# Kernel tuning notes

Hardware: AMD Instinct MI355X
Metric: run time of the kernel (lower is better)

## Reference

```python
import jax, jax.numpy as jnp
import numpy as np

DIM = 8          # per-head dim
ATT_EPS = 1e-15  # LiteMLA eps
BN_EPS = 1e-5    # torch BatchNorm2d default eps


def conv2d(x, w, groups=1, pad=0):
    # x: NCHW, w: OIHW
    return jax.lax.conv_general_dilated(
        x, w, window_strides=(1, 1), padding=[(pad, pad), (pad, pad)],
        dimension_numbers=('NCHW', 'OIHW', 'NCHW'), feature_group_count=groups)


def setup_inputs() -> dict:
    key = jax.random.key(0)
    ks = jax.random.split(key, 6)
    B, C, H, W = 4, 128, 128, 128
    heads = C // DIM            # 16
    t3 = 3 * C                  # 3*total_dim = 384
    x = jax.random.normal(ks[0], (B, C, H, W), jnp.float32)
    w_qkv = jax.random.normal(ks[1], (t3, C, 1, 1), jnp.float32) * 0.02
    w_dw = jax.random.normal(ks[2], (t3, 1, 5, 5), jnp.float32) * 0.02      # depthwise 5x5
    w_pw = jax.random.normal(ks[3], (t3, t3 // (3 * heads), 1, 1), jnp.float32) * 0.05  # grouped 1x1, groups=3*heads
    w_proj = jax.random.normal(ks[4], (C, 2 * C, 1, 1), jnp.float32) * 0.02  # proj 1x1: 2C -> C
    bn_gamma = jnp.ones((C,), jnp.float32)
    bn_beta = jnp.zeros((C,), jnp.float32)
    bn_mean = jnp.zeros((C,), jnp.float32)
    bn_var = jnp.ones((C,), jnp.float32)
    return dict(x=x, w_qkv=w_qkv, w_dw=w_dw, w_pw=w_pw, w_proj=w_proj,
                bn_gamma=bn_gamma, bn_beta=bn_beta, bn_mean=bn_mean, bn_var=bn_var)


def reference(x, w_qkv, w_dw, w_pw, w_proj, bn_gamma, bn_beta, bn_mean, bn_var):
    # qkv: 1x1 conv, no norm / no act
    qkv = conv2d(x, w_qkv)                                  # (B, 3C, H, W)
    t3 = w_qkv.shape[0]
    # aggreg[0]: depthwise 5x5 + grouped 1x1
    groups_pw = t3 // w_pw.shape[1]                         # 3*heads
    agg = conv2d(conv2d(qkv, w_dw, groups=t3, pad=2), w_pw, groups=groups_pw)
    qkv = jnp.concatenate([qkv, agg], axis=1)               # (B, 6C, H, W)

    B, _, H, W = qkv.shape
    N = H * W
    qkv = qkv.reshape(B, -1, 3 * DIM, N)                    # (B, 2*heads, 3*dim, N)
    q = jax.nn.relu(qkv[:, :, :DIM])                        # (B, h, d, N)
    k = jax.nn.relu(qkv[:, :, DIM:2 * DIM])                 # (B, h, d, N)
    v = qkv[:, :, 2 * DIM:]                                 # (B, h, d, N)
    # pad v with a row of ones for normalization
    v = jnp.concatenate([v, jnp.ones_like(v[:, :, :1])], axis=2)  # (B, h, d+1, N)

    vk = jnp.einsum('bhdn,bhen->bhde', v, k)                # (B, h, d+1, d)
    out = jnp.einsum('bhde,bhen->bhdn', vk, q)              # (B, h, d+1, N)
    out = out[:, :, :-1] / (out[:, :, -1:] + ATT_EPS)       # (B, h, d, N)
    out = out.reshape(B, -1, H, W)                          # (B, 2C, H, W)

    # proj: 1x1 conv + BatchNorm2d (inference), no act
    out = conv2d(out, w_proj)                               # (B, C, H, W)
    inv = bn_gamma / jnp.sqrt(bn_var + BN_EPS)
    out = out * inv[:, None, None] + (bn_beta - bn_mean * inv)[:, None, None]
    return out
```

## Files before the change

### kernel.cpp

```cpp
#include <hip/hip_runtime.h>

#define BB 4
#define CIN 128
#define T3 384
#define HH 128
#define WW 128
#define NPIX 16384
#define QKV_ELE (BB*T3*NPIX)
#define NCHUNK 16

#define SEC 4160
#define KGP 1040
#define PLN 520
#define KGPB 520
#define PLNB 260

typedef __attribute__((ext_vector_type(8))) short bf16x8;
typedef __attribute__((ext_vector_type(4))) float f32x4;

__device__ __forceinline__ unsigned splitpack(float x) {
  unsigned u = __float_as_uint(x);
  unsigned hb = (u + 0x7fffu + ((u >> 16) & 1u)) >> 16;
  float lo = x - __uint_as_float(hb << 16);
  unsigned ul = __float_as_uint(lo);
  unsigned lb = (ul + 0x7fffu + ((ul >> 16) & 1u)) >> 16;
  return (hb << 16) | (lb & 0xffffu);
}

__device__ __forceinline__ void packpair(float a, float b, unsigned& hi, unsigned& lo) {
  unsigned p0 = splitpack(a), p1 = splitpack(b);
  hi = (p1 & 0xffff0000u) | (p0 >> 16);
  lo = (p1 << 16) | (p0 & 0xffffu);
}

__global__ __launch_bounds__(256) void k0_wprep(const float* __restrict__ wqkv,
                                                unsigned* __restrict__ wimg,
                                                float* __restrict__ zbuf) {
  int id = blockIdx.x * 256 + threadIdx.x;
  if (id < 16) zbuf[id] = 0.f;
  int i = id & 3;
  int co = (id >> 2) & 127;
  int kgrp = (id >> 9) & 3;
  int c = (id >> 11) & 3;
  int m = id >> 13;
  int ci = c * 32 + kgrp * 8 + 2 * i;
  const float* wrow = wqkv + (size_t)(m * 128 + co) * 128 + ci;
  unsigned hi, lo;
  packpair(wrow[0], wrow[1], hi, lo);
  size_t base = (size_t)(m * 4 + c) * SEC + kgrp * KGP + co * 4 + i;
  wimg[base] = hi;
  wimg[base + PLN] = lo;
}

__global__ __launch_bounds__(256) void k1_qkv_mfma(const float* __restrict__ x,
                                                   const unsigned* __restrict__ wimg,
                                                   float* __restrict__ qkv) {
  __shared__ __align__(16) unsigned Xp[4 * KGP];
  __shared__ __align__(16) unsigned Wp[4 * KGP];
  const int t = threadIdx.x;
  const int p = blockIdx.x;
  const int qd = p / 24;
  const int r_ = p - qd * 24;
  const int m = r_ >> 3;
  const int tt = qd * 8 + (r_ & 7);
  const int n0 = (tt & 127) * 128;
  const int b = tt >> 7;
  const float* xb = x + (size_t)b * CIN * NPIX + n0;

  const int l = t & 63;
  const int w = t >> 6;
  const int g = l >> 4;
  const int lc = l & 15;
  const int ch = w >> 1;
  const int nh = w & 1;
  const int kg = t >> 6;
  const int nn_ = t & 63;

  f32x4 acc[4][4];
  #pragma unroll
  for (int i = 0; i < 4; ++i)
    #pragma unroll
    for (int j = 0; j < 4; ++j) acc[i][j] = (f32x4){0.f, 0.f, 0.f, 0.f};

  uint4 wpre[5];
  float xpre[16];

  {
    const uint4* wsrc = (const uint4*)(wimg + (size_t)(m * 4 + 0) * SEC);
    #pragma unroll
    for (int r = 0; r < 5; ++r) {
      int idx = t + r * 256;
      uint4 v = make_uint4(0u, 0u, 0u, 0u);
      if (idx < 1040) v = wsrc[idx];
      wpre[r] = v;
    }
    const float* colbase = xb + (size_t)(kg * 8) * NPIX;
    #pragma unroll
    for (int half = 0; half < 2; ++half) {
      const float* colp = colbase + nn_ + half * 64;
      #pragma unroll
      for (int i = 0; i < 8; ++i)
        xpre[half * 8 + i] = colp[(size_t)i * NPIX];
    }
  }

  for (int c = 0; c < 4; ++c) {
    {
      uint4* wdst = (uint4*)Wp;
      #pragma unroll
      for (int r = 0; r < 5; ++r) {
        int idx = t + r * 256;
        if (idx < 1040) wdst[idx] = wpre[r];
      }
      #pragma unroll
      for (int half = 0; half < 2; ++half) {
        int n = nn_ + half * 64;
        unsigned hp[4], lp[4];
        #pragma unroll
        for (int i = 0; i < 4; ++i)
          packpair(xpre[half * 8 + 2 * i], xpre[half * 8 + 2 * i + 1], hp[i], lp[i]);
        *(uint4*)&Xp[kg * KGP + n * 4] = make_uint4(hp[0], hp[1], hp[2], hp[3]);
        *(uint4*)&Xp[kg * KGP + PLN + n * 4] = make_uint4(lp[0], lp[1], lp[2], lp[3]);
      }
    }
    __syncthreads();

    if (c < 3) {
      const uint4* wsrc = (const uint4*)(wimg + (size_t)(m * 4 + c + 1) * SEC);
      #pragma unroll
      for (int r = 0; r < 5; ++r) {
        int idx = t + r * 256;
        uint4 v = make_uint4(0u, 0u, 0u, 0u);
        if (idx < 1040) v = wsrc[idx];
        wpre[r] = v;
      }
      const float* colbase = xb + (size_t)((c + 1) * 32 + kg * 8) * NPIX;
      #pragma unroll
      for (int half = 0; half < 2; ++half) {
        const float* colp = colbase + nn_ + half * 64;
        #pragma unroll
        for (int i = 0; i < 8; ++i)
          xpre[half * 8 + i] = colp[(size_t)i * NPIX];
      }
    }

    bf16x8 bh[4], bl[4];
    #pragma unroll
    for (int ng = 0; ng < 4; ++ng) {
      const int nb = (nh * 64 + ng * 16 + lc) * 4;
      bh[ng] = *(const bf16x8*)&Xp[g * KGP + nb];
      bl[ng] = *(const bf16x8*)&Xp[g * KGP + PLN + nb];
    }
    #pragma unroll
    for (int cg = 0; cg < 4; ++cg) {
      const int cb = (ch * 64 + cg * 16 + lc) * 4;
      bf16x8 ah = *(const bf16x8*)&Wp[g * KGP + cb];
      bf16x8 al = *(const bf16x8*)&Wp[g * KGP + PLN + cb];
      #pragma unroll
      for (int ng = 0; ng < 4; ++ng) {
        acc[cg][ng] = __builtin_amdgcn_mfma_f32_16x16x32_bf16(ah, bh[ng], acc[cg][ng], 0, 0, 0);
        acc[cg][ng] = __builtin_amdgcn_mfma_f32_16x16x32_bf16(ah, bl[ng], acc[cg][ng], 0, 0, 0);
        acc[cg][ng] = __builtin_amdgcn_mfma_f32_16x16x32_bf16(al, bh[ng], acc[cg][ng], 0, 0, 0);
      }
    }
    __syncthreads();
  }
  #pragma unroll
  for (int cg = 0; cg < 4; ++cg) {
    const size_t corow = (size_t)b * T3 + m * 128 + ch * 64 + cg * 16 + g * 4;
    #pragma unroll
    for (int ng = 0; ng < 4; ++ng) {
      const int nn = n0 + nh * 64 + ng * 16 + lc;
      #pragma unroll
      for (int rr = 0; rr < 4; ++rr)
        qkv[(corow + rr) * NPIX + nn] = acc[cg][ng][rr];
    }
  }
}

#define PDW 36
__global__ __launch_bounds__(256, 2) void k2_dwpw(const float* __restrict__ qkv,
                                                  const float* __restrict__ wdw,
                                                  const float* __restrict__ wpw,
                                                  const float* __restrict__ zbuf,
                                                  float* __restrict__ agg) {
  __shared__ __align__(16) float dws[8 * 16 * PDW];
  __shared__ float wds[8][25];
  __shared__ float wps[64];
  const int t = threadIdx.x;
  const int p = blockIdx.x;
  const int L = (p & 7) * 768 + (p >> 3);
  const int z = L >> 5;
  const int rem = L & 31;
  const int x0 = (rem & 3) * 32;
  const int y0 = (rem >> 2) * 16;
  const int b = z / 48;
  const int g = z % 48;
  const float* src = qkv + ((size_t)b * T3 + g * 8) * NPIX;

  for (int idx = t; idx < 200; idx += 256)
    wds[idx / 25][idx % 25] = wdw[(size_t)g * 200 + idx];
  if (t < 64) wps[t] = wpw[g * 64 + t];
  __syncthreads();

  const int ch = t >> 5;
  const int xq = t & 7;
  const int yg = (t >> 3) & 3;
  const float* plane = src + (size_t)ch * NPIX;
  const int gx0 = x0 + 4 * xq - 4;
  const bool ex0 = (gx0 >= 0);
  const bool ex2 = (gx0 + 11 < WW);

  f32x4 u[8][3];
  #pragma unroll
  for (int r = 0; r < 8; ++r) {
    const int gy = y0 + 4 * yg - 2 + r;
    const bool iny = (unsigned)gy < (unsigned)HH;
    const float* rp = plane + gy * WW + gx0;
    const float* p0 = (iny && ex0) ? rp : zbuf;
    const float* p1 = iny ? (rp + 4) : zbuf;
    const float* p2 = (iny && ex2) ? (rp + 8) : zbuf;
    u[r][0] = *(const f32x4*)p0;
    u[r][1] = *(const f32x4*)p1;
    u[r][2] = *(const f32x4*)p2;
  }

  float dacc[4][4];
  #pragma unroll
  for (int jy = 0; jy < 4; ++jy)
    #pragma unroll
    for (int jx = 0; jx < 4; ++jx) dacc[jy][jx] = 0.f;

  #pragma unroll
  for (int r = 0; r < 8; ++r) {
    float vals[12] = {u[r][0][0], u[r][0][1], u[r][0][2], u[r][0][3],
                      u[r][1][0], u[r][1][1], u[r][1][2], u[r][1][3],
                      u[r][2][0], u[r][2][1], u[r][2][2], u[r][2][3]};
    #pragma unroll
    for (int jy = 0; jy < 4; ++jy) {
      int ky = r - jy;
      if (ky < 0 || ky > 4) continue;
      #pragma unroll
      for (int kx = 0; kx < 5; ++kx) {
        float wv = wds[ch][ky * 5 + kx];
        #pragma unroll
        for (int jx = 0; jx < 4; ++jx)
          dacc[jy][jx] += wv * vals[jx + kx + 2];
      }
    }
  }

  #pragma unroll
  for (int jy = 0; jy < 4; ++jy) {
    float4 o = make_float4(dacc[jy][0], dacc[jy][1], dacc[jy][2], dacc[jy][3]);
    *(float4*)&dws[ch * (16 * PDW) + (yg * 4 + jy) * PDW + xq * 4] = o;
  }
  __syncthreads();

  float* dst = agg + ((size_t)b * T3 + g * 8) * NPIX + (size_t)y0 * WW + x0;
  #pragma unroll
  for (int pp = 0; pp < 2; ++pp) {
    int pix = t + pp * 256;
    int py = pix >> 5;
    int px = pix & 31;
    float dv[8];
    #pragma unroll
    for (int ic = 0; ic < 8; ++ic) dv[ic] = dws[ic * (16 * PDW) + py * PDW + px];
    #pragma unroll
    for (int oc = 0; oc < 8; ++oc) {
      float s = 0.f;
      #pragma unroll
      for (int ic = 0; ic < 8; ++ic) s += wps[oc * 8 + ic] * dv[ic];
      dst[(size_t)oc * NPIX + py * WW + px] = s;
    }
  }
}

__global__ __launch_bounds__(256) void k3_vk(const float* __restrict__ qkv,
                                             const float* __restrict__ agg,
                                             float* __restrict__ part) {
  const int chunk = blockIdx.x;
  const int bh = blockIdx.y;
  const int b = bh >> 5;
  const int h = bh & 31;
  const int hh = h & 15;
  const float* base = (h < 16 ? qkv : agg) + ((size_t)b * T3 + hh * 24) * NPIX;
  const float* kb = base + 8 * NPIX;
  const float* vb = base + 16 * NPIX;
  const int t = threadIdx.x;
  const int wv = t >> 6;
  const int lane = t & 63;
  const int d0 = wv * 2;

  float accA[8], accB[8], accS[8];
  #pragma unroll
  for (int e = 0; e < 8; ++e) { accA[e] = 0.f; accB[e] = 0.f; accS[e] = 0.f; }

  int p = chunk * (NPIX / NCHUNK) + lane;
  for (int it = 0; it < (NPIX / NCHUNK / 64); ++it, p += 64) {
    float kvv[8];
    #pragma unroll
    for (int e = 0; e < 8; ++e) kvv[e] = fmaxf(kb[(size_t)e * NPIX + p], 0.f);
    float vA = vb[(size_t)d0 * NPIX + p];
    float vB = vb[(size_t)(d0 + 1) * NPIX + p];
    #pragma unroll
    for (int e = 0; e < 8; ++e) { accA[e] += vA * kvv[e]; accB[e] += vB * kvv[e]; }
    if (wv == 0) {
      #pragma unroll
      for (int e = 0; e < 8; ++e) accS[e] += kvv[e];
    }
  }
  #pragma unroll
  for (int e = 0; e < 8; ++e) {
    #pragma unroll
    for (int m = 1; m < 64; m <<= 1) {
      accA[e] += __shfl_xor(accA[e], m);
      accB[e] += __shfl_xor(accB[e], m);
    }
  }
  if (wv == 0) {
    #pragma unroll
    for (int e = 0; e < 8; ++e)
      #pragma unroll
      for (int m = 1; m < 64; m <<= 1) accS[e] += __shfl_xor(accS[e], m);
  }
  if (lane == 0) {
    float* pr = part + ((size_t)bh * NCHUNK + chunk) * 72;
    #pragma unroll
    for (int e = 0; e < 8; ++e) {
      pr[d0 * 8 + e] = accA[e];
      pr[(d0 + 1) * 8 + e] = accB[e];
    }
    if (wv == 0) {
      #pragma unroll
      for (int e = 0; e < 8; ++e) pr[64 + e] = accS[e];
    }
  }
}

__global__ __launch_bounds__(128) void k3b_sum(const float* __restrict__ part,
                                               float* __restrict__ vk) {
  const int bh = blockIdx.x;
  const int j = threadIdx.x;
  if (j < 72) {
    float s = 0.f;
    #pragma unroll
    for (int c = 0; c < NCHUNK; ++c) s += part[((size_t)bh * NCHUNK + c) * 72 + j];
    vk[(size_t)bh * 72 + j] = s;
  }
}

__global__ __launch_bounds__(256) void k3c_M(const float* __restrict__ wproj,
                                             const float* __restrict__ vk,
                                             const float* __restrict__ gamma,
                                             const float* __restrict__ beta,
                                             const float* __restrict__ mean,
                                             const float* __restrict__ var,
                                             unsigned* __restrict__ Mimg,
                                             float* __restrict__ shiftb) {
  int id = blockIdx.x * 256 + threadIdx.x;
  int i = id & 3;
  int co = (id >> 2) & 127;
  int kgrp = (id >> 9) & 3;
  int cidx = (id >> 11) & 7;
  int b = id >> 14;
  int h = cidx * 4 + kgrp;
  float inv = gamma[co] * rsqrtf(var[co] + 1e-5f);
  const float* wrow = wproj + (size_t)co * 256 + h * 8;
  const float* vkc = vk + ((size_t)b * 32 + h) * 72;
  float s0 = 0.f, s1 = 0.f;
  #pragma unroll
  for (int d = 0; d < 8; ++d) {
    float wv = wrow[d];
    s0 += wv * vkc[d * 8 + 2 * i];
    s1 += wv * vkc[d * 8 + 2 * i + 1];
  }
  unsigned hi, lo;
  packpair(inv * s0, inv * s1, hi, lo);
  size_t base = (size_t)(b * 8 + cidx) * SEC + kgrp * KGP + co * 4 + i;
  Mimg[base] = hi;
  Mimg[base + PLN] = lo;
  if (b == 0 && cidx == 0 && kgrp == 0 && i == 0)
    shiftb[co] = beta[co] - mean[co] * inv;
}

__global__ __launch_bounds__(256) void k4_mfma(const float* __restrict__ qkv,
                                               const float* __restrict__ agg,
                                               const float* __restrict__ vk,
                                               const unsigned* __restrict__ Mimg,
                                               const float* __restrict__ shiftb,
                                               float* __restrict__ out) {
  __shared__ __align__(16) unsigned Ap[4 * KGP];
  __shared__ __align__(16) unsigned Bp[4 * KGPB];
  const int t = threadIdx.x;
  const int n0 = blockIdx.x * 64;
  const int b = blockIdx.y;

  const int l = t & 63;
  const int w = t >> 6;
  const int g = l >> 4;
  const int lc = l & 15;
  const int ch = w >> 1;
  const int nh = w & 1;
  const int hj = t >> 6;
  const int nn_ = t & 63;

  f32x4 acc[4][2];
  #pragma unroll
  for (int i = 0; i < 4; ++i)
    #pragma unroll
    for (int j = 0; j < 2; ++j) acc[i][j] = (f32x4){0.f, 0.f, 0.f, 0.f};

  uint4 apre[5];
  float qpre[8];
  float vv[8];

  {
    const uint4* asrc = (const uint4*)(Mimg + (size_t)(b * 8 + 0) * SEC);
    #pragma unroll
    for (int r = 0; r < 5; ++r) {
      int idx = t + r * 256;
      uint4 v = make_uint4(0u, 0u, 0u, 0u);
      if (idx < 1040) v = asrc[idx];
      apre[r] = v;
    }
    const int h = hj;
    const float* srcb = (h < 16 ? qkv : agg) +
                        ((size_t)b * T3 + (h & 15) * 24) * NPIX + n0 + nn_;
    const float* vkr = vk + ((size_t)b * 32 + h) * 72 + 64;
    #pragma unroll
    for (int e = 0; e < 8; ++e) {
      qpre[e] = srcb[(size_t)e * NPIX];
      vv[e] = vkr[e];
    }
  }

  for (int cidx = 0; cidx < 8; ++cidx) {
    {
      uint4* adst = (uint4*)Ap;
      #pragma unroll
      for (int r = 0; r < 5; ++r) {
        int idx = t + r * 256;
        if (idx < 1040) adst[idx] = apre[r];
      }
    }
    {
      float q[8];
      float den = 1e-15f;
      #pragma unroll
      for (int e = 0; e < 8; ++e) {
        q[e] = fmaxf(qpre[e], 0.f);
        den += vv[e] * q[e];
      }
      float rd = 1.0f / den;
      unsigned hp[4], lp[4];
      #pragma unroll
      for (int i = 0; i < 4; ++i)
        packpair(q[2 * i] * rd, q[2 * i + 1] * rd, hp[i], lp[i]);
      *(uint4*)&Bp[hj * KGPB + nn_ * 4] = make_uint4(hp[0], hp[1], hp[2], hp[3]);
      *(uint4*)&Bp[hj * KGPB + PLNB + nn_ * 4] = make_uint4(lp[0], lp[1], lp[2], lp[3]);
    }
    __syncthreads();

    if (cidx < 7) {
      const uint4* asrc = (const uint4*)(Mimg + (size_t)(b * 8 + cidx + 1) * SEC);
      #pragma unroll
      for (int r = 0; r < 5; ++r) {
        int idx = t + r * 256;
        uint4 v = make_uint4(0u, 0u, 0u, 0u);
        if (idx < 1040) v = asrc[idx];
        apre[r] = v;
      }
      const int h = (cidx + 1) * 4 + hj;
      const float* srcb = (h < 16 ? qkv : agg) +
                          ((size_t)b * T3 + (h & 15) * 24) * NPIX + n0 + nn_;
      const float* vkr = vk + ((size_t)b * 32 + h) * 72 + 64;
      #pragma unroll
      for (int e = 0; e < 8; ++e) {
        qpre[e] = srcb[(size_t)e * NPIX];
        vv[e] = vkr[e];
      }
    }

    bf16x8 bhf[2], blf[2];
    #pragma unroll
    for (int ng = 0; ng < 2; ++ng) {
      const int nb = (nh * 32 + ng * 16 + lc) * 4;
      bhf[ng] = *(const bf16x8*)&Bp[g * KGPB + nb];
      blf[ng] = *(const bf16x8*)&Bp[g * KGPB + PLNB + nb];
    }
    #pragma unroll
    for (int cg = 0; cg < 4; ++cg) {
      const int cb = (ch * 64 + cg * 16 + lc) * 4;
      bf16x8 ah = *(const bf16x8*)&Ap[g * KGP + cb];
      bf16x8 al = *(const bf16x8*)&Ap[g * KGP + PLN + cb];
      #pragma unroll
      for (int ng = 0; ng < 2; ++ng) {
        acc[cg][ng] = __builtin_amdgcn_mfma_f32_16x16x32_bf16(ah, bhf[ng], acc[cg][ng], 0, 0, 0);
        acc[cg][ng] = __builtin_amdgcn_mfma_f32_16x16x32_bf16(ah, blf[ng], acc[cg][ng], 0, 0, 0);
        acc[cg][ng] = __builtin_amdgcn_mfma_f32_16x16x32_bf16(al, bhf[ng], acc[cg][ng], 0, 0, 0);
      }
    }
    __syncthreads();
  }
  #pragma unroll
  for (int cg = 0; cg < 4; ++cg) {
    const int cobase = ch * 64 + cg * 16 + g * 4;
    #pragma unroll
    for (int ng = 0; ng < 2; ++ng) {
      const int nn = n0 + nh * 32 + ng * 16 + lc;
      #pragma unroll
      for (int rr = 0; rr < 4; ++rr) {
        int co = cobase + rr;
        out[((size_t)b * 128 + co) * NPIX + nn] = acc[cg][ng][rr] + shiftb[co];
      }
    }
  }
}

__global__ void fill_sentinel(float* o, int n) {
  int i = blockIdx.x * 256 + threadIdx.x;
  if (i < n) o[i] = 12345.0f;
}

extern "C" void kernel_launch(void* const* d_in, const int* in_sizes, int n_in,
                              void* d_out, int out_size, void* d_ws, size_t ws_size,
                              hipStream_t stream) {
  const float* x     = (const float*)d_in[0];
  const float* wqkv  = (const float*)d_in[1];
  const float* wdw   = (const float*)d_in[2];
  const float* wpw   = (const float*)d_in[3];
  const float* wproj = (const float*)d_in[4];
  const float* gamma = (const float*)d_in[5];
  const float* beta  = (const float*)d_in[6];
  const float* mean  = (const float*)d_in[7];
  const float* var   = (const float*)d_in[8];
  float* out = (float*)d_out;
  float* ws = (float*)d_ws;

  const size_t partF = 128 * NCHUNK * 72;
  const size_t mimgF = 32 * SEC;
  const size_t wimgF = 12 * SEC;
  const size_t needF = (size_t)QKV_ELE * 2 + partF + 9216 + 128 + mimgF + wimgF + 16;
  if (ws_size < needF * 4) {
    fill_sentinel<<<dim3((out_size + 255) / 256), dim3(256), 0, stream>>>(out, out_size);
    return;
  }
  float* qkv    = ws;
  float* agg    = qkv + QKV_ELE;
  float* part   = agg + QKV_ELE;
  float* vkbuf  = part + partF;
  float* shiftb = vkbuf + 9216;
  unsigned* Mimg = (unsigned*)(shiftb + 128);
  unsigned* wimg = Mimg + mimgF;
  float* zbuf   = (float*)(wimg + wimgF);

  k0_wprep<<<dim3(96), 256, 0, stream>>>(wqkv, wimg, zbuf);
  k1_qkv_mfma<<<dim3(1536), 256, 0, stream>>>(x, wimg, qkv);
  k2_dwpw<<<dim3(6144), 256, 0, stream>>>(qkv, wdw, wpw, zbuf, agg);
  k3_vk<<<dim3(NCHUNK, 128), 256, 0, stream>>>(qkv, agg, part);
  k3b_sum<<<dim3(128), 128, 0, stream>>>(part, vkbuf);
  k3c_M<<<dim3(256), 256, 0, stream>>>(wproj, vkbuf, gamma, beta, mean, var, Mimg, shiftb);
  k4_mfma<<<dim3(256, 4), 256, 0, stream>>>(qkv, agg, vkbuf, Mimg, shiftb, out);
}
```

Measured before the change: 134.7 us.

## Merge raw-qkv VK reduction blocks into depthwise/pointwise kernel launch

The K^T V reduction for the 16 heads that read raw qkv no longer depends on the aggregation output, so those 1024 blocks now run inside the depthwise+pointwise kernel's grid alongside its 6144 conv blocks. The separate VK kernel is left with only the 64x16 blocks over the aggregated heads. This shortens the launch chain and lets the memory-bound reduction overlap with the conv work. In exchange, the fused kernel carries the conv kernel's shared memory and launch bounds for every block, and block-index interleaving decides how the two kinds of work spread across CUs.

```diff
diff --git a/kernel.cpp b/kernel.cpp
--- a/kernel.cpp
+++ b/kernel.cpp
@@ -178,18 +178,88 @@
   }
 }
 
+__device__ __forceinline__ void k3_body(const float* __restrict__ base,
+                                        float* __restrict__ part,
+                                        int chunk, int bh, int t) {
+  const float* kb = base + 8 * NPIX;
+  const float* vb = base + 16 * NPIX;
+  const int wv = t >> 6;
+  const int lane = t & 63;
+  const int d0 = wv * 2;
+
+  float accA[8], accB[8], accS[8];
+  #pragma unroll
+  for (int e = 0; e < 8; ++e) { accA[e] = 0.f; accB[e] = 0.f; accS[e] = 0.f; }
+
+  int p = chunk * (NPIX / NCHUNK) + lane;
+  for (int it = 0; it < (NPIX / NCHUNK / 64); ++it, p += 64) {
+    float kvv[8];
+    #pragma unroll
+    for (int e = 0; e < 8; ++e) kvv[e] = fmaxf(kb[(size_t)e * NPIX + p], 0.f);
+    float vA = vb[(size_t)d0 * NPIX + p];
+    float vB = vb[(size_t)(d0 + 1) * NPIX + p];
+    #pragma unroll
+    for (int e = 0; e < 8; ++e) { accA[e] += vA * kvv[e]; accB[e] += vB * kvv[e]; }
+    if (wv == 0) {
+      #pragma unroll
+      for (int e = 0; e < 8; ++e) accS[e] += kvv[e];
+    }
+  }
+  #pragma unroll
+  for (int e = 0; e < 8; ++e) {
+    #pragma unroll
+    for (int m = 1; m < 64; m <<= 1) {
+      accA[e] += __shfl_xor(accA[e], m);
+      accB[e] += __shfl_xor(accB[e], m);
+    }
+  }
+  if (wv == 0) {
+    #pragma unroll
+    for (int e = 0; e < 8; ++e)
+      #pragma unroll
+      for (int m = 1; m < 64; m <<= 1) accS[e] += __shfl_xor(accS[e], m);
+  }
+  if (lane == 0) {
+    float* pr = part + ((size_t)bh * NCHUNK + chunk) * 72;
+    #pragma unroll
+    for (int e = 0; e < 8; ++e) {
+      pr[d0 * 8 + e] = accA[e];
+      pr[(d0 + 1) * 8 + e] = accB[e];
+    }
+    if (wv == 0) {
+      #pragma unroll
+      for (int e = 0; e < 8; ++e) pr[64 + e] = accS[e];
+    }
+  }
+}
+
 #define PDW 36
-__global__ __launch_bounds__(256, 2) void k2_dwpw(const float* __restrict__ qkv,
-                                                  const float* __restrict__ wdw,
-                                                  const float* __restrict__ wpw,
-                                                  const float* __restrict__ zbuf,
-                                                  float* __restrict__ agg) {
+__global__ __launch_bounds__(256, 2) void k2_fat(const float* __restrict__ qkv,
+                                                 const float* __restrict__ wdw,
+                                                 const float* __restrict__ wpw,
+                                                 const float* __restrict__ zbuf,
+                                                 float* __restrict__ agg,
+                                                 float* __restrict__ part) {
   __shared__ __align__(16) float dws[8 * 16 * PDW];
   __shared__ float wds[8][25];
   __shared__ float wps[64];
   const int t = threadIdx.x;
-  const int p = blockIdx.x;
-  const int L = (p & 7) * 768 + (p >> 3);
+  const int id = blockIdx.x;
+  const int r_ = id & 7;
+  const int o_ = id >> 3;
+
+  if (o_ < 128) {
+    const int q = r_ * 128 + o_;
+    const int chunk = q & 15;
+    const int bhq = q >> 4;
+    const int b = bhq >> 4;
+    const int h = bhq & 15;
+    const float* base = qkv + ((size_t)b * T3 + h * 24) * NPIX;
+    k3_body(base, part, chunk, b * 32 + h, t);
+    return;
+  }
+
+  const int L = r_ * 768 + (o_ - 128);
   const int z = L >> 5;
   const int rem = L & 31;
   const int x0 = (rem & 3) * 32;
@@ -276,66 +346,14 @@
   }
 }
 
-__global__ __launch_bounds__(256) void k3_vk(const float* __restrict__ qkv,
-                                             const float* __restrict__ agg,
-                                             float* __restrict__ part) {
+__global__ __launch_bounds__(256) void k3_agg(const float* __restrict__ agg,
+                                              float* __restrict__ part) {
   const int chunk = blockIdx.x;
-  const int bh = blockIdx.y;
-  const int b = bh >> 5;
-  const int h = bh & 31;
-  const int hh = h & 15;
-  const float* base = (h < 16 ? qkv : agg) + ((size_t)b * T3 + hh * 24) * NPIX;
-  const float* kb = base + 8 * NPIX;
-  const float* vb = base + 16 * NPIX;
-  const int t = threadIdx.x;
-  const int wv = t >> 6;
-  const int lane = t & 63;
-  const int d0 = wv * 2;
-
-  float accA[8], accB[8], accS[8];
-  #pragma unroll
-  for (int e = 0; e < 8; ++e) { accA[e] = 0.f; accB[e] = 0.f; accS[e] = 0.f; }
-
-  int p = chunk * (NPIX / NCHUNK) + lane;
-  for (int it = 0; it < (NPIX / NCHUNK / 64); ++it, p += 64) {
-    float kvv[8];
-    #pragma unroll
-    for (int e = 0; e < 8; ++e) kvv[e] = fmaxf(kb[(size_t)e * NPIX + p], 0.f);
-    float vA = vb[(size_t)d0 * NPIX + p];
-    float vB = vb[(size_t)(d0 + 1) * NPIX + p];
-    #pragma unroll
-    for (int e = 0; e < 8; ++e) { accA[e] += vA * kvv[e]; accB[e] += vB * kvv[e]; }
-    if (wv == 0) {
-      #pragma unroll
-      for (int e = 0; e < 8; ++e) accS[e] += kvv[e];
-    }
-  }
-  #pragma unroll
-  for (int e = 0; e < 8; ++e) {
-    #pragma unroll
-    for (int m = 1; m < 64; m <<= 1) {
-      accA[e] += __shfl_xor(accA[e], m);
-      accB[e] += __shfl_xor(accB[e], m);
-    }
-  }
-  if (wv == 0) {
-    #pragma unroll
-    for (int e = 0; e < 8; ++e)
-      #pragma unroll
-      for (int m = 1; m < 64; m <<= 1) accS[e] += __shfl_xor(accS[e], m);
-  }
-  if (lane == 0) {
-    float* pr = part + ((size_t)bh * NCHUNK + chunk) * 72;
-    #pragma unroll
-    for (int e = 0; e < 8; ++e) {
-      pr[d0 * 8 + e] = accA[e];
-      pr[(d0 + 1) * 8 + e] = accB[e];
-    }
-    if (wv == 0) {
-      #pragma unroll
-      for (int e = 0; e < 8; ++e) pr[64 + e] = accS[e];
-    }
-  }
+  const int bhq = blockIdx.y;
+  const int b = bhq >> 4;
+  const int hh = bhq & 15;
+  const float* base = agg + ((size_t)b * T3 + hh * 24) * NPIX;
+  k3_body(base, part, chunk, b * 32 + 16 + hh, threadIdx.x);
 }
 
 __global__ __launch_bounds__(128) void k3b_sum(const float* __restrict__ part,
@@ -557,8 +575,8 @@
 
   k0_wprep<<<dim3(96), 256, 0, stream>>>(wqkv, wimg, zbuf);
   k1_qkv_mfma<<<dim3(1536), 256, 0, stream>>>(x, wimg, qkv);
-  k2_dwpw<<<dim3(6144), 256, 0, stream>>>(qkv, wdw, wpw, zbuf, agg);
-  k3_vk<<<dim3(NCHUNK, 128), 256, 0, stream>>>(qkv, agg, part);
+  k2_fat<<<dim3(7168), 256, 0, stream>>>(qkv, wdw, wpw, zbuf, agg, part);
+  k3_agg<<<dim3(16, 64), 256, 0, stream>>>(agg, part);
   k3b_sum<<<dim3(128), 128, 0, stream>>>(part, vkbuf);
   k3c_M<<<dim3(256), 256, 0, stream>>>(wproj, vkbuf, gamma, beta, mean, var, Mimg, shiftb);
   k4_mfma<<<dim3(256, 4), 256, 0, stream>>>(qkv, agg, vkbuf, Mimg, shiftb, out);
```

Measured after the change: 135.9 us. Within noise of the previous version (+0.9%).
